# Performance work log

Measured on AMD Instinct MI355X. Metric: run time of the kernel, lower is better.

## Reference

```python
import jax, jax.numpy as jnp
import numpy as np

B, IN_DIM, OUT_DIM, FAN_IN = 1024, 4096, 4096, 8

def setup_inputs() -> dict:
    key = jax.random.key(0)
    k1, k2, k3 = jax.random.split(key, 3)
    x = jax.random.normal(k1, (B, IN_DIM), dtype=jnp.float32)
    # fixed random fan-in connectivity (out_dim, fan_in), values in [0, in_dim)
    idx = jax.random.randint(k2, (OUT_DIM, FAN_IN), 0, IN_DIM, dtype=jnp.int64)
    # xavier_uniform for (out_dim, fan_in)
    limit = np.sqrt(6.0 / (OUT_DIM + FAN_IN))
    w = jax.random.uniform(k3, (OUT_DIM, FAN_IN), minval=-limit, maxval=limit, dtype=jnp.float32)
    # theta_init = 'mean_abs_w': mean |w| per row * fan_in/2
    theta = jnp.abs(w).mean(axis=1) * (FAN_IN / 2.0)
    s_raw = jnp.full((OUT_DIM,), 1.0, dtype=jnp.float32)
    return {"x": x, "idx": idx, "w": w, "theta": theta, "s_raw": s_raw}

def reference(x, idx, w, theta, s_raw):
    # gather fan-in inputs: (B, out_dim, fan_in)
    x_sel = x[:, idx]
    # weighted reduce over fan_in, subtract threshold
    z = jnp.einsum('bof,of->bo', x_sel, w) - theta[None, :]
    s = jax.nn.softplus(s_raw) + 1e-6  # positive slope
    return jax.nn.sigmoid(s[None, :] * z)
```

## Files before the change

kernel.cpp:

```cpp
#include <hip/hip_runtime.h>
#include <hip/hip_fp16.h>
#include <math.h>

#define BDIM 1024
#define IN_DIM 4096
#define OUT_DIM 4096
#define FAN_IN 8
#define NT 1024
#define TILE_B 4
#define OPT (OUT_DIM / NT)

#define LOG2E 1.442695040888963f
#define LN2   0.6931471805599453f

__device__ __forceinline__ float fast_exp(float v) {
    return exp2f(v * LOG2E);
}

union H2U { __half2 h; unsigned int u; };

__global__ __launch_bounds__(NT, 4) void WeightedThresholdGate_53085795778563_kernel(
    const float* __restrict__ x,
    const int*   __restrict__ idx,
    const float* __restrict__ w,
    const float* __restrict__ theta,
    const float* __restrict__ s_raw,
    float*       __restrict__ out)
{
    __shared__ __align__(8) uint2 xT[IN_DIM];

    const int t  = threadIdx.x;
    const int b0 = blockIdx.x * TILE_B;

    const float* __restrict__ xr0 = x + (size_t)(b0 + 0) * IN_DIM;
    const float* __restrict__ xr1 = x + (size_t)(b0 + 1) * IN_DIM;
    const float* __restrict__ xr2 = x + (size_t)(b0 + 2) * IN_DIM;
    const float* __restrict__ xr3 = x + (size_t)(b0 + 3) * IN_DIM;

#pragma unroll
    for (int k = 0; k < IN_DIM / NT; ++k) {
        const int j = t + k * NT;
        H2U lo, hi;
        lo.h = __floats2half2_rn(xr0[j], xr1[j]);
        hi.h = __floats2half2_rn(xr2[j], xr3[j]);
        xT[j] = make_uint2(lo.u, hi.u);
    }
    __syncthreads();

#pragma unroll
    for (int i = 0; i < OPT; ++i) {
        const int o = t + i * NT;

        const int4*   ip = reinterpret_cast<const int4*>(idx + (size_t)o * FAN_IN);
        const float4* wp = reinterpret_cast<const float4*>(w  + (size_t)o * FAN_IN);
        const int4   i0 = ip[0], i1 = ip[1];
        const float4 w0 = wp[0], w1 = wp[1];

        float a0 = 0.f, a1 = 0.f, a2 = 0.f, a3 = 0.f;

#define GATHER(J, WF)                                              \
        {                                                          \
            const uint2 g = xT[(J)];                               \
            H2U glo, ghi; glo.u = g.x; ghi.u = g.y;                \
            const float2 f01 = __half22float2(glo.h);              \
            const float2 f23 = __half22float2(ghi.h);              \
            a0 = fmaf(f01.x, (WF), a0);                            \
            a1 = fmaf(f01.y, (WF), a1);                            \
            a2 = fmaf(f23.x, (WF), a2);                            \
            a3 = fmaf(f23.y, (WF), a3);                            \
        }

        GATHER(i0.x, w0.x); GATHER(i0.y, w0.y);
        GATHER(i0.z, w0.z); GATHER(i0.w, w0.w);
        GATHER(i1.x, w1.x); GATHER(i1.y, w1.y);
        GATHER(i1.z, w1.z); GATHER(i1.w, w1.w);
#undef GATHER

        const float th = theta[o];
        const float sr = s_raw[o];
        const float sp = fmaxf(sr, 0.0f) + LN2 * log2f(1.0f + fast_exp(-fabsf(sr)));
        const float s  = sp + 1e-6f;

        const float g0 = 1.0f / (1.0f + fast_exp(-s * (a0 - th)));
        const float g1 = 1.0f / (1.0f + fast_exp(-s * (a1 - th)));
        const float g2 = 1.0f / (1.0f + fast_exp(-s * (a2 - th)));
        const float g3 = 1.0f / (1.0f + fast_exp(-s * (a3 - th)));

        __builtin_nontemporal_store(g0, &out[(size_t)(b0 + 0) * OUT_DIM + o]);
        __builtin_nontemporal_store(g1, &out[(size_t)(b0 + 1) * OUT_DIM + o]);
        __builtin_nontemporal_store(g2, &out[(size_t)(b0 + 2) * OUT_DIM + o]);
        __builtin_nontemporal_store(g3, &out[(size_t)(b0 + 3) * OUT_DIM + o]);
    }
}

extern "C" void kernel_launch(void* const* d_in, const int* in_sizes, int n_in,
                              void* d_out, int out_size, void* d_ws, size_t ws_size,
                              hipStream_t stream) {
    const float* x     = (const float*)d_in[0];
    const int*   idx   = (const int*)  d_in[1];
    const float* w     = (const float*)d_in[2];
    const float* theta = (const float*)d_in[3];
    const float* s_raw = (const float*)d_in[4];
    float* out = (float*)d_out;

    dim3 grid(BDIM / TILE_B);
    dim3 block(NT);
    WeightedThresholdGate_53085795778563_kernel<<<grid, block, 0, stream>>>(
        x, idx, w, theta, s_raw, out);
}
```

Measured before the change: 13.85 us.

## Vectorize x loads and output stores by assigning four contiguous outputs per thread

```diff
diff --git a/kernel.cpp b/kernel.cpp
--- a/kernel.cpp
+++ b/kernel.cpp
@@ -8,10 +8,12 @@
 #define FAN_IN 8
 #define NT 1024
 #define TILE_B 4
-#define OPT (OUT_DIM / NT)
+#define OPT 4
 
 #define LOG2E 1.442695040888963f
 #define LN2   0.6931471805599453f
+
+typedef float f32x4 __attribute__((ext_vector_type(4)));
 
 __device__ __forceinline__ float fast_exp(float v) {
     return exp2f(v * LOG2E);
@@ -27,29 +29,44 @@
     const float* __restrict__ s_raw,
     float*       __restrict__ out)
 {
-    __shared__ __align__(8) uint2 xT[IN_DIM];
+    __shared__ __align__(16) uint2 xT[IN_DIM];
 
     const int t  = threadIdx.x;
     const int b0 = blockIdx.x * TILE_B;
 
-    const float* __restrict__ xr0 = x + (size_t)(b0 + 0) * IN_DIM;
-    const float* __restrict__ xr1 = x + (size_t)(b0 + 1) * IN_DIM;
-    const float* __restrict__ xr2 = x + (size_t)(b0 + 2) * IN_DIM;
-    const float* __restrict__ xr3 = x + (size_t)(b0 + 3) * IN_DIM;
-
+    {
+        const float4* __restrict__ xv0 = reinterpret_cast<const float4*>(x + (size_t)(b0 + 0) * IN_DIM);
+        const float4* __restrict__ xv1 = reinterpret_cast<const float4*>(x + (size_t)(b0 + 1) * IN_DIM);
+        const float4* __restrict__ xv2 = reinterpret_cast<const float4*>(x + (size_t)(b0 + 2) * IN_DIM);
+        const float4* __restrict__ xv3 = reinterpret_cast<const float4*>(x + (size_t)(b0 + 3) * IN_DIM);
+        const float4 r0 = xv0[t];
+        const float4 r1 = xv1[t];
+        const float4 r2 = xv2[t];
+        const float4 r3 = xv3[t];
+        const float e0[4] = {r0.x, r0.y, r0.z, r0.w};
+        const float e1[4] = {r1.x, r1.y, r1.z, r1.w};
+        const float e2[4] = {r2.x, r2.y, r2.z, r2.w};
+        const float e3[4] = {r3.x, r3.y, r3.z, r3.w};
 #pragma unroll
-    for (int k = 0; k < IN_DIM / NT; ++k) {
-        const int j = t + k * NT;
-        H2U lo, hi;
-        lo.h = __floats2half2_rn(xr0[j], xr1[j]);
-        hi.h = __floats2half2_rn(xr2[j], xr3[j]);
-        xT[j] = make_uint2(lo.u, hi.u);
+        for (int jj = 0; jj < 4; ++jj) {
+            H2U lo, hi;
+            lo.h = __floats2half2_rn(e0[jj], e1[jj]);
+            hi.h = __floats2half2_rn(e2[jj], e3[jj]);
+            xT[4 * t + jj] = make_uint2(lo.u, hi.u);
+        }
     }
     __syncthreads();
 
+    const float4 th4 = reinterpret_cast<const float4*>(theta)[t];
+    const float4 sr4 = reinterpret_cast<const float4*>(s_raw)[t];
+    const float  thv[4] = {th4.x, th4.y, th4.z, th4.w};
+    const float  srv[4] = {sr4.x, sr4.y, sr4.z, sr4.w};
+
+    float g[OPT][TILE_B];
+
 #pragma unroll
     for (int i = 0; i < OPT; ++i) {
-        const int o = t + i * NT;
+        const int o = 4 * t + i;
 
         const int4*   ip = reinterpret_cast<const int4*>(idx + (size_t)o * FAN_IN);
         const float4* wp = reinterpret_cast<const float4*>(w  + (size_t)o * FAN_IN);
@@ -60,8 +77,8 @@
 
 #define GATHER(J, WF)                                              \
         {                                                          \
-            const uint2 g = xT[(J)];                               \
-            H2U glo, ghi; glo.u = g.x; ghi.u = g.y;                \
+            const uint2 gg = xT[(J)];                              \
+            H2U glo, ghi; glo.u = gg.x; ghi.u = gg.y;              \
             const float2 f01 = __half22float2(glo.h);              \
             const float2 f23 = __half22float2(ghi.h);              \
             a0 = fmaf(f01.x, (WF), a0);                            \
@@ -76,20 +93,23 @@
         GATHER(i1.z, w1.z); GATHER(i1.w, w1.w);
 #undef GATHER
 
-        const float th = theta[o];
-        const float sr = s_raw[o];
+        const float sr = srv[i];
         const float sp = fmaxf(sr, 0.0f) + LN2 * log2f(1.0f + fast_exp(-fabsf(sr)));
         const float s  = sp + 1e-6f;
+        const float th = thv[i];
 
-        const float g0 = 1.0f / (1.0f + fast_exp(-s * (a0 - th)));
-        const float g1 = 1.0f / (1.0f + fast_exp(-s * (a1 - th)));
-        const float g2 = 1.0f / (1.0f + fast_exp(-s * (a2 - th)));
-        const float g3 = 1.0f / (1.0f + fast_exp(-s * (a3 - th)));
+        g[i][0] = 1.0f / (1.0f + fast_exp(-s * (a0 - th)));
+        g[i][1] = 1.0f / (1.0f + fast_exp(-s * (a1 - th)));
+        g[i][2] = 1.0f / (1.0f + fast_exp(-s * (a2 - th)));
+        g[i][3] = 1.0f / (1.0f + fast_exp(-s * (a3 - th)));
+    }
 
-        __builtin_nontemporal_store(g0, &out[(size_t)(b0 + 0) * OUT_DIM + o]);
-        __builtin_nontemporal_store(g1, &out[(size_t)(b0 + 1) * OUT_DIM + o]);
-        __builtin_nontemporal_store(g2, &out[(size_t)(b0 + 2) * OUT_DIM + o]);
-        __builtin_nontemporal_store(g3, &out[(size_t)(b0 + 3) * OUT_DIM + o]);
+#pragma unroll
+    for (int r = 0; r < TILE_B; ++r) {
+        f32x4 v;
+        v.x = g[0][r]; v.y = g[1][r]; v.z = g[2][r]; v.w = g[3][r];
+        f32x4* orow = reinterpret_cast<f32x4*>(out + (size_t)(b0 + r) * OUT_DIM);
+        __builtin_nontemporal_store(v, &orow[t]);
     }
 }
 
```

Result: slower. 20.97 us (+51.4%).
